# Optimization experiments

Hardware: AMD Instinct MI355X
Metric: run time of the kernel (lower is better)

The kernel has to match this reference:

```python
import jax, jax.numpy as jnp
import numpy as np

EPS = 1e-8
MASK_FILL = 1000000000.0  # value used to disable dropped codes


def _normalize(x):
    return x / (jnp.linalg.norm(x, ord=2, axis=-1, keepdims=True) + EPS)


def setup_inputs() -> dict:
    key = jax.random.key(0)
    k_x, k_cb, k_mask = jax.random.split(key, 3)
    B, K, D = 16384, 16384, 64
    dropout = 0.1
    x = jax.random.normal(k_x, (B, D), dtype=jnp.float32)
    # lecun_uniform init for the codebook param: U(-l, l), l = sqrt(3 / fan_in)
    lim = np.sqrt(3.0 / D).astype(np.float32)
    codebook = jax.random.uniform(k_cb, (K, D), dtype=jnp.float32, minval=-lim, maxval=lim)
    mask = jax.random.bernoulli(k_mask, p=1.0 - dropout, shape=(B, K))
    return {"x": x, "codebook": codebook, "mask": mask, "training": 1}


def reference(x, codebook, mask, training):
    # setup(): codebook param is normalized once at construction
    cb = _normalize(codebook)                       # [K, d]
    # __call__():
    x_n = _normalize(x)                             # [b, d]
    cb_n = _normalize(cb)                           # normalized again in __call__
    distance = -jnp.matmul(x_n, cb_n.T)             # [b, K] negative cosine sim
    if training:
        distance = jnp.where(mask, distance, MASK_FILL)
    indices = jnp.argmin(distance, axis=-1)         # [b]
    z = cb[indices]                                 # gather from once-normalized codebook
    z_q = x_n + jax.lax.stop_gradient(z - x_n)      # straight-through estimator
    return (z_q, z, x_n, indices)
```

## Files before the change

### kernel.cpp

```cpp
#include <hip/hip_runtime.h>
#include <math.h>
#include <float.h>

#define EPSV 1e-8f
constexpr int D = 64;

typedef __attribute__((ext_vector_type(8)))  short short8;
typedef __attribute__((ext_vector_type(16))) float f32x16;

static __device__ __forceinline__ unsigned short f2bf(float f) {
    unsigned u = __float_as_uint(f);
    unsigned r = u + 0x7FFFu + ((u >> 16) & 1u);
    return (unsigned short)(r >> 16);
}
static __device__ __forceinline__ float bf2f(unsigned short b) {
    return __uint_as_float(((unsigned)b) << 16);
}
static __device__ __forceinline__ unsigned umin2(unsigned a, unsigned b) { return a < b ? a : b; }
static __device__ __forceinline__ unsigned umax2(unsigned a, unsigned b) { return a > b ? a : b; }

static __device__ __forceinline__ size_t fragidx(int e, int k) {
    return (size_t)(e >> 5) * 2048 + (size_t)(k >> 3) * 256 + (e & 31) * 8 + (k & 7);
}

__global__ __launch_bounds__(256) void k_prep_cb(const float* __restrict__ cbin,
                                                 float* __restrict__ cb,
                                                 unsigned short* __restrict__ ch,
                                                 unsigned short* __restrict__ cl) {
    const int t = threadIdx.x;
    const int wv = t >> 6, lane = t & 63;
    const int code = blockIdx.x * 4 + wv;
    float v = cbin[(size_t)code * D + lane];
    float ss = v * v;
    #pragma unroll
    for (int off = 32; off; off >>= 1) ss += __shfl_xor(ss, off, 64);
    const float c1 = v / (sqrtf(ss) + EPSV);
    cb[(size_t)code * D + lane] = c1;
    float ss2 = c1 * c1;
    #pragma unroll
    for (int off = 32; off; off >>= 1) ss2 += __shfl_xor(ss2, off, 64);
    const float c2 = c1 / (sqrtf(ss2) + EPSV);
    const unsigned short h = f2bf(c2);
    const size_t fi = fragidx(code, lane);
    ch[fi] = h;
    cl[fi] = f2bf(c2 - bf2f(h));
}

__global__ __launch_bounds__(256) void k_prep_x(const float* __restrict__ xin,
                                                float* __restrict__ xn,
                                                unsigned short* __restrict__ xh,
                                                unsigned short* __restrict__ xl,
                                                int* __restrict__ fixcnt) {
    const int t = threadIdx.x;
    if (blockIdx.x == 0 && t == 0) *fixcnt = 0;
    const int wv = t >> 6, lane = t & 63;
    const int row = blockIdx.x * 4 + wv;
    float v = xin[(size_t)row * D + lane];
    float ss = v * v;
    #pragma unroll
    for (int off = 32; off; off >>= 1) ss += __shfl_xor(ss, off, 64);
    const float xv = v / (sqrtf(ss) + EPSV);
    xn[(size_t)row * D + lane] = xv;
    const unsigned short h = f2bf(xv);
    const size_t fi = fragidx(row, lane);
    xh[fi] = h;
    xl[fi] = f2bf(xv - bf2f(h));
}

__global__ __launch_bounds__(256, 4) void k_mfma(const unsigned short* __restrict__ xh,
                                                 const unsigned short* __restrict__ xl,
                                                 const unsigned short* __restrict__ ch,
                                                 const unsigned short* __restrict__ cl,
                                                 unsigned* __restrict__ pk1,
                                                 unsigned* __restrict__ pk2,
                                                 int B, int K) {
    const int t = threadIdx.x;
    const int wv = t >> 6, lane = t & 63;
    const int lh = lane >> 5, lm = lane & 31;
    const int ks = (int)(blockIdx.x & 7);
    const int rb = (int)(blockIdx.x >> 3);
    const int lh4 = lh * 4;

    const short8* xh8 = (const short8*)xh;
    const short8* xl8 = (const short8*)xl;
    const short8* ch8 = (const short8*)ch;
    const short8* cl8 = (const short8*)cl;

    const int rp = rb * 4 + wv;
    const int row = rp * 32 + lm;

    short8 bh[4], bl[4];
    #pragma unroll
    for (int s = 0; s < 4; ++s) {
        const size_t bi = (size_t)rp * 256 + (s * 2 + lh) * 32 + lm;
        bh[s] = xh8[bi];
        bl[s] = xl8[bi];
    }

    unsigned k1 = 0xFFFFFFFFu, k2 = 0xFFFFFFFFu;

    #pragma unroll 1
    for (int tt = 0; tt < 32; ++tt) {
        const int ct = ks * 32 + tt;
        #pragma unroll
        for (int p = 0; p < 2; ++p) {
            const int cp = ct * 2 + p;
            short8 ah[4], al[4];
            #pragma unroll
            for (int s = 0; s < 4; ++s) {
                const size_t ai = (size_t)cp * 256 + (s * 2 + lh) * 32 + lm;
                ah[s] = ch8[ai];
                al[s] = cl8[ai];
            }
            f32x16 acc;
            #pragma unroll
            for (int i = 0; i < 16; ++i) acc[i] = 0.f;
            #pragma unroll
            for (int s = 0; s < 4; ++s) {
                acc = __builtin_amdgcn_mfma_f32_32x32x16_bf16(ah[s], bh[s], acc, 0, 0, 0);
                acc = __builtin_amdgcn_mfma_f32_32x32x16_bf16(ah[s], bl[s], acc, 0, 0, 0);
                acc = __builtin_amdgcn_mfma_f32_32x32x16_bf16(al[s], bh[s], acc, 0, 0, 0);
            }
            const unsigned kbase = (unsigned)(ct * 64 + p * 32 + lh4);
            #pragma unroll
            for (int r = 0; r < 16; ++r) {
                const int base = (r & 3) + 8 * (r >> 2);
                const float qf = fmaf(acc[r], -65536.0f, 131072.0f);
                const unsigned key = ((unsigned)(int)qf << 14) | kbase | (unsigned)base;
                k2 = umin2(k2, umax2(k1, key));
                k1 = umin2(k1, key);
            }
        }
    }

    const unsigned o1 = (unsigned)__shfl_xor((int)k1, 32, 64);
    const unsigned o2 = (unsigned)__shfl_xor((int)k2, 32, 64);
    const unsigned mx = umax2(k1, o1);
    k1 = umin2(k1, o1);
    k2 = umin2(umin2(k2, o2), mx);

    if (lh == 0) {
        pk1[(size_t)ks * B + row] = k1;
        pk2[(size_t)ks * B + row] = k2;
    }
}

__global__ __launch_bounds__(256) void k_comb(const unsigned* __restrict__ pk1,
                                              const unsigned* __restrict__ pk2,
                                              const int* __restrict__ mask,
                                              const int* __restrict__ training,
                                              const float* __restrict__ xn,
                                              const float* __restrict__ cb,
                                              float* __restrict__ out,
                                              int* __restrict__ fixlist,
                                              int* __restrict__ fixcnt,
                                              int B, int K) {
    const int t = threadIdx.x;
    const int wv = t >> 6, lane = t & 63;
    const int row = blockIdx.x * 4 + wv;
    const int tr = training[0];

    unsigned cand = 0xFFFFFFFFu;
    int m = 1;
    if (lane < 16) {
        const int c = lane & 7;
        cand = (lane < 8) ? pk1[(size_t)c * B + row] : pk2[(size_t)c * B + row];
        m = (tr == 0) ? 1 : mask[(size_t)row * K + (cand & 16383u)];
    }
    const unsigned eff = (lane < 16 && m != 0) ? cand : 0xFFFFFFFFu;

    unsigned b1 = eff, b2 = 0xFFFFFFFFu;
    #pragma unroll
    for (int off = 1; off < 16; off <<= 1) {
        const unsigned oa = (unsigned)__shfl_xor((int)b1, off, 16);
        const unsigned ob = (unsigned)__shfl_xor((int)b2, off, 16);
        const unsigned mx = umax2(b1, oa);
        b1 = umin2(b1, oa);
        b2 = umin2(umin2(b2, ob), mx);
    }
    const unsigned best   = (unsigned)__shfl((int)b1, 0, 64);
    const unsigned second = (unsigned)__shfl((int)b2, 0, 64);
    const unsigned long long lim = (unsigned long long)best + (10ull << 14);

    const int mo        = __shfl_xor(m, 8, 16);
    const unsigned a2v  = (unsigned)__shfl_xor((int)cand, 8, 16);
    const bool cflag = (lane < 8) && (m == 0) && (mo == 0) &&
                       ((unsigned long long)a2v < lim);
    const bool flag = __any(cflag) ||
                      (best == 0xFFFFFFFFu) ||
                      ((unsigned long long)second < lim);

    const int bi = (int)(best & 16383u);
    const float zv  = cb[(size_t)bi * D + lane];
    const float xnv = xn[(size_t)row * D + lane];
    out[(size_t)row * D + lane] = xnv + (zv - xnv);
    out[(size_t)B * D + (size_t)row * D + lane] = zv;
    if (lane == 0) {
        out[(size_t)3 * B * D + row] = (float)bi;
        if (flag) {
            const int p = atomicAdd(fixcnt, 1);
            fixlist[p] = row;
        }
    }
}

__global__ __launch_bounds__(256) void k_fix(const float* __restrict__ xn,
                                             const float* __restrict__ cb,
                                             const int* __restrict__ mask,
                                             const int* __restrict__ training,
                                             const int* __restrict__ fixlist,
                                             const int* __restrict__ fixcnt,
                                             float* __restrict__ out, int B, int K) {
    const int nf = *fixcnt;
    const int tr = training[0];
    __shared__ float sv[256];
    __shared__ int   si[256];
    const int t = threadIdx.x;
    for (int i = blockIdx.x; i < nf; i += gridDim.x) {
        const int row = fixlist[i];
        const float* xr = xn + (size_t)row * D;
        float b1 = FLT_MAX; int i1 = 0;
        for (int k = t; k < K; k += 256) {
            const float* cr = cb + (size_t)k * D;
            float s = 0.f;
            #pragma unroll
            for (int d = 0; d < D; ++d) s = fmaf(xr[d], cr[d], s);
            const int m = mask[(size_t)row * K + k];
            const float dist = (tr && m == 0) ? 1000000000.0f : -s;
            if (dist < b1) { b1 = dist; i1 = k; }
        }
        sv[t] = b1; si[t] = i1;
        __syncthreads();
        for (int s = 128; s; s >>= 1) {
            if (t < s) {
                const float ov = sv[t + s]; const int oi = si[t + s];
                if (ov < sv[t] || (ov == sv[t] && oi < si[t])) { sv[t] = ov; si[t] = oi; }
            }
            __syncthreads();
        }
        const int bi = si[0];
        if (t < 64) {
            const float zv  = cb[(size_t)bi * D + t];
            const float xnv = xr[t];
            out[(size_t)row * D + t] = xnv + (zv - xnv);
            out[(size_t)B * D + (size_t)row * D + t] = zv;
        }
        if (t == 0) out[(size_t)3 * B * D + row] = (float)bi;
        __syncthreads();
    }
}

extern "C" void kernel_launch(void* const* d_in, const int* in_sizes, int n_in,
                              void* d_out, int out_size, void* d_ws, size_t ws_size,
                              hipStream_t stream) {
    const float* x    = (const float*)d_in[0];
    const float* cbin = (const float*)d_in[1];
    const int* mask   = (const int*)d_in[2];
    const int* train  = (const int*)d_in[3];
    const int B = in_sizes[0] / D;
    const int K = in_sizes[1] / D;
    float* out = (float*)d_out;
    float* out_xn = out + (size_t)2 * B * D;

    char* w = (char*)d_ws;
    float* cbw          = (float*)w;
    unsigned short* xhw = (unsigned short*)(w + (size_t)K * D * 4);
    unsigned short* xlw = xhw + (size_t)B * D;
    unsigned short* chw = xlw + (size_t)B * D;
    unsigned short* clw = chw + (size_t)K * D;
    unsigned* pk1       = (unsigned*)(clw + (size_t)K * D);
    unsigned* pk2       = pk1 + (size_t)B * 8;
    int* fixlist        = (int*)(pk2 + (size_t)B * 8);
    int* fixcnt         = fixlist + B;

    k_prep_cb<<<K / 4, 256, 0, stream>>>(cbin, cbw, chw, clw);
    k_prep_x <<<B / 4, 256, 0, stream>>>(x, out_xn, xhw, xlw, fixcnt);
    k_mfma   <<<(B / 128) * 8, 256, 0, stream>>>(xhw, xlw, chw, clw, pk1, pk2, B, K);
    k_comb   <<<B / 4, 256, 0, stream>>>(pk1, pk2, mask, train, out_xn, cbw, out,
                                         fixlist, fixcnt, B, K);
    k_fix    <<<256, 256, 0, stream>>>(out_xn, cbw, mask, train, fixlist, fixcnt,
                                       out, B, K);
}
```

Before: 252.3 us.

## Stage codebook tiles in LDS with double-buffered async loads; merge prep kernels

The MFMA kernel now copies each codebook tile (hi and lo bf16 fragments) into shared memory using async global-to-LDS loads, double-buffered, and prefetches the next tile while computing the current one. Before, all four waves read the same codebook fragments from global memory directly. This is meant to cut redundant global/L2 traffic and hide load latency. The two prep kernels are also merged into one launch to save launch overhead. The cost is a block-wide barrier per tile, 32 KB of LDS per block that may reduce occupancy, and reliance on the async load completing before the barrier.

```diff
diff --git a/kernel.cpp b/kernel.cpp
--- a/kernel.cpp
+++ b/kernel.cpp
@@ -23,48 +23,48 @@
     return (size_t)(e >> 5) * 2048 + (size_t)(k >> 3) * 256 + (e & 31) * 8 + (k & 7);
 }
 
-__global__ __launch_bounds__(256) void k_prep_cb(const float* __restrict__ cbin,
-                                                 float* __restrict__ cb,
-                                                 unsigned short* __restrict__ ch,
-                                                 unsigned short* __restrict__ cl) {
-    const int t = threadIdx.x;
-    const int wv = t >> 6, lane = t & 63;
-    const int code = blockIdx.x * 4 + wv;
-    float v = cbin[(size_t)code * D + lane];
-    float ss = v * v;
-    #pragma unroll
-    for (int off = 32; off; off >>= 1) ss += __shfl_xor(ss, off, 64);
-    const float c1 = v / (sqrtf(ss) + EPSV);
-    cb[(size_t)code * D + lane] = c1;
-    float ss2 = c1 * c1;
-    #pragma unroll
-    for (int off = 32; off; off >>= 1) ss2 += __shfl_xor(ss2, off, 64);
-    const float c2 = c1 / (sqrtf(ss2) + EPSV);
-    const unsigned short h = f2bf(c2);
-    const size_t fi = fragidx(code, lane);
-    ch[fi] = h;
-    cl[fi] = f2bf(c2 - bf2f(h));
-}
-
-__global__ __launch_bounds__(256) void k_prep_x(const float* __restrict__ xin,
-                                                float* __restrict__ xn,
-                                                unsigned short* __restrict__ xh,
-                                                unsigned short* __restrict__ xl,
-                                                int* __restrict__ fixcnt) {
+__global__ __launch_bounds__(256) void k_prep(const float* __restrict__ cbin,
+                                              float* __restrict__ cb,
+                                              unsigned short* __restrict__ ch,
+                                              unsigned short* __restrict__ cl,
+                                              const float* __restrict__ xin,
+                                              float* __restrict__ xn,
+                                              unsigned short* __restrict__ xh,
+                                              unsigned short* __restrict__ xl,
+                                              int* __restrict__ fixcnt,
+                                              int nbcb) {
     const int t = threadIdx.x;
     if (blockIdx.x == 0 && t == 0) *fixcnt = 0;
     const int wv = t >> 6, lane = t & 63;
-    const int row = blockIdx.x * 4 + wv;
-    float v = xin[(size_t)row * D + lane];
-    float ss = v * v;
-    #pragma unroll
-    for (int off = 32; off; off >>= 1) ss += __shfl_xor(ss, off, 64);
-    const float xv = v / (sqrtf(ss) + EPSV);
-    xn[(size_t)row * D + lane] = xv;
-    const unsigned short h = f2bf(xv);
-    const size_t fi = fragidx(row, lane);
-    xh[fi] = h;
-    xl[fi] = f2bf(xv - bf2f(h));
+    if ((int)blockIdx.x < nbcb) {
+        const int code = blockIdx.x * 4 + wv;
+        float v = cbin[(size_t)code * D + lane];
+        float ss = v * v;
+        #pragma unroll
+        for (int off = 32; off; off >>= 1) ss += __shfl_xor(ss, off, 64);
+        const float c1 = v / (sqrtf(ss) + EPSV);
+        cb[(size_t)code * D + lane] = c1;
+        float ss2 = c1 * c1;
+        #pragma unroll
+        for (int off = 32; off; off >>= 1) ss2 += __shfl_xor(ss2, off, 64);
+        const float c2 = c1 / (sqrtf(ss2) + EPSV);
+        const unsigned short h = f2bf(c2);
+        const size_t fi = fragidx(code, lane);
+        ch[fi] = h;
+        cl[fi] = f2bf(c2 - bf2f(h));
+    } else {
+        const int row = (blockIdx.x - nbcb) * 4 + wv;
+        float v = xin[(size_t)row * D + lane];
+        float ss = v * v;
+        #pragma unroll
+        for (int off = 32; off; off >>= 1) ss += __shfl_xor(ss, off, 64);
+        const float xv = v / (sqrtf(ss) + EPSV);
+        xn[(size_t)row * D + lane] = xv;
+        const unsigned short h = f2bf(xv);
+        const size_t fi = fragidx(row, lane);
+        xh[fi] = h;
+        xl[fi] = f2bf(xv - bf2f(h));
+    }
 }
 
 __global__ __launch_bounds__(256, 4) void k_mfma(const unsigned short* __restrict__ xh,
@@ -74,6 +74,8 @@
                                                  unsigned* __restrict__ pk1,
                                                  unsigned* __restrict__ pk2,
                                                  int B, int K) {
+    __shared__ short8 lch[2][2][256];
+    __shared__ short8 lcl[2][2][256];
     const int t = threadIdx.x;
     const int wv = t >> 6, lane = t & 63;
     const int lh = lane >> 5, lm = lane & 31;
@@ -97,20 +99,45 @@
         bl[s] = xl8[bi];
     }
 
+#define STAGE(b_, tt_) do {                                                    \
+    const int ct_ = ks * 32 + (tt_);                                           \
+    const short8* s0 = ch8 + (size_t)(ct_ * 2 + 0) * 256 + t;                  \
+    const short8* s1 = ch8 + (size_t)(ct_ * 2 + 1) * 256 + t;                  \
+    const short8* s2 = cl8 + (size_t)(ct_ * 2 + 0) * 256 + t;                  \
+    const short8* s3 = cl8 + (size_t)(ct_ * 2 + 1) * 256 + t;                  \
+    __builtin_amdgcn_global_load_lds(                                          \
+        (const __attribute__((address_space(1))) void*)s0,                     \
+        (__attribute__((address_space(3))) void*)(&lch[b_][0][wv * 64]), 16, 0, 0); \
+    __builtin_amdgcn_global_load_lds(                                          \
+        (const __attribute__((address_space(1))) void*)s1,                     \
+        (__attribute__((address_space(3))) void*)(&lch[b_][1][wv * 64]), 16, 0, 0); \
+    __builtin_amdgcn_global_load_lds(                                          \
+        (const __attribute__((address_space(1))) void*)s2,                     \
+        (__attribute__((address_space(3))) void*)(&lcl[b_][0][wv * 64]), 16, 0, 0); \
+    __builtin_amdgcn_global_load_lds(                                          \
+        (const __attribute__((address_space(1))) void*)s3,                     \
+        (__attribute__((address_space(3))) void*)(&lcl[b_][1][wv * 64]), 16, 0, 0); \
+} while (0)
+
     unsigned k1 = 0xFFFFFFFFu, k2 = 0xFFFFFFFFu;
+
+    STAGE(0, 0);
 
     #pragma unroll 1
     for (int tt = 0; tt < 32; ++tt) {
+        __syncthreads();
+        if (tt < 31) STAGE((tt + 1) & 1, tt + 1);
+        const int bsel = tt & 1;
         const int ct = ks * 32 + tt;
+
         #pragma unroll
         for (int p = 0; p < 2; ++p) {
-            const int cp = ct * 2 + p;
             short8 ah[4], al[4];
             #pragma unroll
             for (int s = 0; s < 4; ++s) {
-                const size_t ai = (size_t)cp * 256 + (s * 2 + lh) * 32 + lm;
-                ah[s] = ch8[ai];
-                al[s] = cl8[ai];
+                const int ai = (s * 2 + lh) * 32 + lm;
+                ah[s] = lch[bsel][p][ai];
+                al[s] = lcl[bsel][p][ai];
             }
             f32x16 acc;
             #pragma unroll
@@ -132,6 +159,7 @@
             }
         }
     }
+#undef STAGE
 
     const unsigned o1 = (unsigned)__shfl_xor((int)k1, 32, 64);
     const unsigned o2 = (unsigned)__shfl_xor((int)k2, 32, 64);
@@ -273,11 +301,11 @@
     int* fixlist        = (int*)(pk2 + (size_t)B * 8);
     int* fixcnt         = fixlist + B;
 
-    k_prep_cb<<<K / 4, 256, 0, stream>>>(cbin, cbw, chw, clw);
-    k_prep_x <<<B / 4, 256, 0, stream>>>(x, out_xn, xhw, xlw, fixcnt);
-    k_mfma   <<<(B / 128) * 8, 256, 0, stream>>>(xhw, xlw, chw, clw, pk1, pk2, B, K);
-    k_comb   <<<B / 4, 256, 0, stream>>>(pk1, pk2, mask, train, out_xn, cbw, out,
-                                         fixlist, fixcnt, B, K);
-    k_fix    <<<256, 256, 0, stream>>>(out_xn, cbw, mask, train, fixlist, fixcnt,
-                                       out, B, K);
-}
+    k_prep <<<K / 4 + B / 4, 256, 0, stream>>>(cbin, cbw, chw, clw,
+                                               x, out_xn, xhw, xlw, fixcnt, K / 4);
+    k_mfma <<<(B / 128) * 8, 256, 0, stream>>>(xhw, xlw, chw, clw, pk1, pk2, B, K);
+    k_comb <<<B / 4, 256, 0, stream>>>(pk1, pk2, mask, train, out_xn, cbw, out,
+                                       fixlist, fixcnt, B, K);
+    k_fix  <<<256, 256, 0, stream>>>(out_xn, cbw, mask, train, fixlist, fixcnt,
+                                     out, B, K);
+}
```

Result: faster. 238.1 us, median of 2 (-5.7%).
